# Optimization experiments

Measured on AMD Instinct MI355X. Metric: run time of the kernel, lower is better.

Reference implementation:

```python
import jax, jax.numpy as jnp
import numpy as np

N = 8192      # nodes
E = 131072    # edges (avg degree 16)
MUL = 128     # multiplicity of 0e and 1o channels
A = 10        # node_attrs (element one-hot) dim
RB = 8        # radial basis size
INV_SQRT3 = 0.5773502691896258  # w3j normalization for l=1 paths


def _lin0(x, W):
    # e3nn-style Linear on scalar (l=0) channels, 1/sqrt(fan_in) normalization
    return (x @ W) / jnp.sqrt(jnp.asarray(W.shape[0], x.dtype))


def _lin1(v, W):
    # e3nn-style Linear on l=1 channels: mixes multiplicities, acts identically on the 3 components
    return jnp.einsum('nuc,uw->nwc', v, W) / jnp.sqrt(jnp.asarray(W.shape[0], v.dtype))


def setup_inputs() -> dict:
    key = jax.random.key(0)
    ks = jax.random.split(key, 26)
    f32 = jnp.float32
    w = lambda k, s: jax.random.normal(k, s, f32)
    D_EF = RB + 2 * MUL  # 264: radial basis + source + target scalar embeddings
    return {
        'node_attrs': jax.random.uniform(ks[0], (N, A), f32),
        'node_feats': w(ks[1], (N, 4 * MUL)),
        'edge_attrs': w(ks[2], (E, 4)),
        'edge_feats': jax.random.uniform(ks[3], (E, RB), f32),
        'edge_index': jax.random.randint(ks[4], (2, E), 0, N, jnp.int32),
        'W_skip_s': w(ks[5], (MUL, MUL)), 'W_skip_v': w(ks[6], (MUL, MUL)),
        'W_up_s': w(ks[7], (MUL, MUL)), 'W_up_v': w(ks[8], (MUL, MUL)),
        'W_src': w(ks[9], (A, MUL)), 'W_tgt': w(ks[10], (A, MUL)),
        'W_r0': w(ks[11], (D_EF, 64)), 'W_r1': w(ks[12], (64, 64)),
        'W_r2': w(ks[13], (64, 64)), 'W_r3': w(ks[14], (64, 4 * MUL)),
        'W_d0': w(ks[15], (D_EF, 64)), 'W_d1': w(ks[16], (64, 1)),
        'W1_s': w(ks[17], (2 * MUL, 2 * MUL)), 'W1_v': w(ks[18], (2 * MUL, MUL)),
        'Wres_s': w(ks[19], (MUL, 2 * MUL)), 'Wres_v': w(ks[20], (MUL, MUL)),
        'W2_s': w(ks[21], (MUL, MUL)), 'W2_v': w(ks[22], (MUL, MUL)),
        'alpha': jnp.asarray(20.0, f32), 'beta': jnp.asarray(0.0, f32),
    }


def reference(node_attrs, node_feats, edge_attrs, edge_feats, edge_index,
              W_skip_s, W_skip_v, W_up_s, W_up_v, W_src, W_tgt,
              W_r0, W_r1, W_r2, W_r3, W_d0, W_d1,
              W1_s, W1_v, Wres_s, Wres_v, W2_s, W2_v, alpha, beta):
    n = node_feats.shape[0]
    s = node_feats[:, :MUL]                       # [N,128] 0e
    v = node_feats[:, MUL:].reshape(n, MUL, 3)    # [N,128,3] 1o
    # skip_tp: Linear(node_feats -> hidden)
    sc = jnp.concatenate([_lin0(s, W_skip_s), _lin1(v, W_skip_v).reshape(n, -1)], axis=-1)
    # linear_up: Linear(node_feats -> edge_irreps)
    us, uv = _lin0(s, W_up_s), _lin1(v, W_up_v)
    # source/target scalar embeddings from node_attrs
    src_e = _lin0(node_attrs, W_src)
    tgt_e = _lin0(node_attrs, W_tgt)
    snd, rcv = edge_index[0], edge_index[1]
    ef = jnp.concatenate([edge_feats, src_e[snd], tgt_e[rcv]], axis=-1)   # [E,264]
    # radial MLP -> per-edge tensor product weights
    h = jax.nn.silu(_lin0(ef, W_r0))
    h = jax.nn.silu(_lin0(h, W_r1))
    h = jax.nn.silu(_lin0(h, W_r2))
    tpw = _lin0(h, W_r3)                          # [E, 4*128]
    # edge density -> per-node density via scatter-sum
    d = jax.nn.silu(_lin0(ef, W_d0))
    edge_density = jnp.tanh(_lin0(d, W_d1) ** 2)  # [E,1]
    density = jax.ops.segment_sum(edge_density, rcv, num_segments=n)      # [N,1]
    # sparse CG tensor product (uvu), paths: 0x0->0e, 0x1->1o, 1x0->1o, 1x1->0e
    xs, xv = us[snd], uv[snd]                     # gather sender features
    y0, y1 = edge_attrs[:, 0], edge_attrs[:, 1:4]
    w1, w2, w3, w4 = jnp.split(tpw, 4, axis=-1)
    m0a = w1 * xs * y0[:, None]                                          # 0e x 0e -> 0e
    m0b = w4 * jnp.einsum('euc,ec->eu', xv, y1) * INV_SQRT3              # 1o x 1o -> 0e
    m1a = (w2 * xs)[:, :, None] * y1[:, None, :] * INV_SQRT3             # 0e x 1o -> 1o
    m1b = w3[:, :, None] * xv * y0[:, None, None] * INV_SQRT3            # 1o x 0e -> 1o
    mid_s = jnp.concatenate([m0a, m0b], axis=1)   # [E,256] irreps_mid scalars
    mid_v = jnp.concatenate([m1a, m1b], axis=1)   # [E,256,3] irreps_mid vectors
    msg_s = jax.ops.segment_sum(mid_s, rcv, num_segments=n)
    msg_v = jax.ops.segment_sum(mid_v, rcv, num_segments=n)
    # linear_1 + learned density normalization
    denom = density * beta + alpha                # [N,1]
    m_s = _lin0(msg_s, W1_s) / denom
    m_v = _lin1(msg_v, W1_v) / denom[..., None]
    # linear_res on up-projected node feats
    m_s = m_s + _lin0(us, Wres_s)                 # [N,256]: 128 scalars + 128 gates
    m_v = m_v + _lin1(uv, Wres_v)                 # [N,128,3]
    # Gate: silu on scalars, sigmoid gates on vectors
    out_s = jax.nn.silu(m_s[:, :MUL])
    out_v = m_v * jax.nn.sigmoid(m_s[:, MUL:])[:, :, None]
    # linear_2
    f_s = _lin0(out_s, W2_s)
    f_v = _lin1(out_v, W2_v)
    # reshape_irreps -> [N, mul, 1+3]
    out = jnp.concatenate([f_s[:, :, None], f_v], axis=2)
    return out, sc
```

## Files before the change

kernel.cpp:

```cpp
#include <hip/hip_runtime.h>

#define NN 8192
#define EE 131072
#define MUL 128
#define AA 10
#define RB 8
#define DEF 264
#define INV_SQRT3 0.5773502691896258f
#define INV_SQRT128 0.08838834764831845f
#define INV_SQRT10 0.31622776601683794f
#define INV_SQRT264 0.06154574548966636f

typedef __attribute__((ext_vector_type(8))) short short8;
typedef __attribute__((ext_vector_type(4))) float floatx4;

#define WS_XQ     ((size_t)0)
#define WS_USB    (WS_XQ    + (size_t)NN*256)
#define WS_UVB    (WS_USB   + (size_t)NN*64)
#define WS_SRC    (WS_UVB   + (size_t)NN*192)
#define WS_TGT    (WS_SRC   + (size_t)NN*64)
#define WS_MSGSB  (WS_TGT   + (size_t)NN*64)
#define WS_MSGVB  (WS_MSGSB + (size_t)NN*128)
#define WS_GATE   (WS_MSGVB + (size_t)NN*384)
#define WS_COUNTS (WS_GATE  + (size_t)NN*128)
#define WS_OFFS   (WS_COUNTS+ (size_t)NN)
#define WS_CURSOR (WS_OFFS  + (size_t)(NN+4))
#define WS_POS    (WS_CURSOR+ (size_t)NN)
#define WS_META   (WS_POS   + (size_t)EE)
#define WS_TPW    (WS_META  + (size_t)EE*8)
#define WS_WB     (WS_TPW   + (size_t)EE*256)
#define WS_WP     (WS_WB    + (size_t)152*256)
#define WS_WN     (WS_WP    + (size_t)352*256)

__device__ __forceinline__ float silu_f(float x) {
    return x * __builtin_amdgcn_rcpf(1.f + __expf(-x));
}
__device__ __forceinline__ float sigm_f(float x) {
    return __builtin_amdgcn_rcpf(1.f + __expf(-x));
}

__device__ __forceinline__ unsigned short f2bf(float x) {
    union { float f; unsigned u; } uf; uf.f = x;
    unsigned r = uf.u + 0x7FFFu + ((uf.u >> 16) & 1u);
    return (unsigned short)(r >> 16);
}

__global__ __launch_bounds__(256) void csr_count(
    const int* __restrict__ edge_index, int* __restrict__ counts)
{
    int e = blockIdx.x * 256 + threadIdx.x;
    atomicAdd(&counts[edge_index[EE + e]], 1);
}

__global__ __launch_bounds__(1024) void csr_scan(
    const int* __restrict__ counts, int* __restrict__ offs, int* __restrict__ cursor)
{
    __shared__ int sums[1024];
    const int t = threadIdx.x;
    int local[8];
    int s = 0;
#pragma unroll
    for (int k = 0; k < 8; ++k) { local[k] = s; s += counts[t * 8 + k]; }
    sums[t] = s;
    __syncthreads();
    for (int d = 1; d < 1024; d <<= 1) {
        int v = (t >= d) ? sums[t - d] : 0;
        __syncthreads();
        sums[t] += v;
        __syncthreads();
    }
    int base = (t > 0) ? sums[t - 1] : 0;
#pragma unroll
    for (int k = 0; k < 8; ++k) {
        offs[t * 8 + k] = base + local[k];
        cursor[t * 8 + k] = base + local[k];
    }
    if (t == 1023) offs[8192] = sums[1023];
}

__global__ __launch_bounds__(256) void csr_scatter(
    const int* __restrict__ edge_index, int* __restrict__ cursor, int* __restrict__ pos)
{
    int e = blockIdx.x * 256 + threadIdx.x;
    pos[e] = atomicAdd(&cursor[edge_index[EE + e]], 1);
}

__global__ __launch_bounds__(256) void swizzle_weights(
    const float* __restrict__ Wr0, const float* __restrict__ Wd0,
    const float* __restrict__ Wr1, const float* __restrict__ Wr2,
    const float* __restrict__ Wr3, unsigned short* __restrict__ WBall)
{
    int fid = blockIdx.x * 256 + threadIdx.x;
    int lane = fid & 63;
    int frag = fid >> 6;
    int k0 = (lane >> 4) * 8;
    int n0 = lane & 15;
    unsigned short o[8];

    if (frag < 72) {
        int kt = frag >> 3, nt = frag & 7;
        int n = nt * 16 + n0;
#pragma unroll
        for (int j = 0; j < 8; ++j) {
            int k = kt * 32 + k0 + j;
            float v = 0.f;
            if (k < 264) v = ((n < 64) ? Wr0[k * 64 + n] : Wd0[k * 64 + (n - 64)]) * INV_SQRT264;
            o[j] = f2bf(v);
        }
    } else if (frag < 80) {
        int fl = frag - 72;
        int kt = fl >> 2, nt = fl & 3;
        int n = nt * 16 + n0;
#pragma unroll
        for (int j = 0; j < 8; ++j)
            o[j] = f2bf(Wr1[(kt * 32 + k0 + j) * 64 + n] * 0.125f);
    } else if (frag < 88) {
        int fl = frag - 80;
        int kt = fl >> 2, nt = fl & 3;
        int n = nt * 16 + n0;
#pragma unroll
        for (int j = 0; j < 8; ++j)
            o[j] = f2bf(Wr2[(kt * 32 + k0 + j) * 64 + n] * 0.125f);
    } else {
        int fl = frag - 88;
        int kt = fl >> 5, nt = fl & 31;
        int n = nt * 16 + n0;
        int q = n >> 6;
        float sc = (q < 2) ? 0.125f : 0.125f * INV_SQRT3;
#pragma unroll
        for (int j = 0; j < 8; ++j)
            o[j] = f2bf(Wr3[(kt * 32 + k0 + j) * 512 + n] * sc);
    }
    uint4 pk;
    pk.x = (unsigned)o[0] | ((unsigned)o[1] << 16);
    pk.y = (unsigned)o[2] | ((unsigned)o[3] << 16);
    pk.z = (unsigned)o[4] | ((unsigned)o[5] << 16);
    pk.w = (unsigned)o[6] | ((unsigned)o[7] << 16);
    *(uint4*)(WBall + (size_t)fid * 8) = pk;
}

__global__ __launch_bounds__(256) void swizzle_post(
    const float* __restrict__ W1s, const float* __restrict__ W1v,
    const float* __restrict__ Wrs, const float* __restrict__ Wrv,
    const float* __restrict__ W2s, const float* __restrict__ W2v,
    unsigned short* __restrict__ WPall)
{
    int fid = blockIdx.x * 256 + threadIdx.x;
    int lane = fid & 63;
    int frag = fid >> 6;
    int k0 = (lane >> 4) * 8;
    int n0 = lane & 15;
    unsigned short o[8];

    if (frag < 192) {
        int kt = frag >> 4, nt = frag & 15;
        int n = nt * 16 + n0;
#pragma unroll
        for (int j = 0; j < 8; ++j) {
            int k = kt * 32 + k0 + j;
            float v = (k < 256) ? W1s[k * 256 + n] * 0.0625f
                                : Wrs[(k - 256) * 256 + n] * INV_SQRT128;
            o[j] = f2bf(v);
        }
    } else if (frag < 288) {
        int fl = frag - 192;
        int kt = fl >> 3, nt = fl & 7;
        int n = nt * 16 + n0;
#pragma unroll
        for (int j = 0; j < 8; ++j) {
            int k = kt * 32 + k0 + j;
            float v = (k < 256) ? W1v[k * 128 + n] * 0.0625f
                                : Wrv[(k - 256) * 128 + n] * INV_SQRT128;
            o[j] = f2bf(v);
        }
    } else if (frag < 320) {
        int fl = frag - 288;
        int kt = fl >> 3, nt = fl & 7;
        int n = nt * 16 + n0;
#pragma unroll
        for (int j = 0; j < 8; ++j)
            o[j] = f2bf(W2s[(kt * 32 + k0 + j) * 128 + n] * INV_SQRT128);
    } else {
        int fl = frag - 320;
        int kt = fl >> 3, nt = fl & 7;
        int n = nt * 16 + n0;
#pragma unroll
        for (int j = 0; j < 8; ++j)
            o[j] = f2bf(W2v[(kt * 32 + k0 + j) * 128 + n] * INV_SQRT128);
    }
    uint4 pk;
    pk.x = (unsigned)o[0] | ((unsigned)o[1] << 16);
    pk.y = (unsigned)o[2] | ((unsigned)o[3] << 16);
    pk.z = (unsigned)o[4] | ((unsigned)o[5] << 16);
    pk.w = (unsigned)o[6] | ((unsigned)o[7] << 16);
    *(uint4*)(WPall + (size_t)fid * 8) = pk;
}

__global__ __launch_bounds__(256) void swizzle_node(
    const float* __restrict__ Wss, const float* __restrict__ Wus,
    const float* __restrict__ Wsv, const float* __restrict__ Wuv,
    const float* __restrict__ Wsrc, const float* __restrict__ Wtgt,
    unsigned short* __restrict__ WN)
{
    int fid = blockIdx.x * 256 + threadIdx.x;
    int lane = fid & 63;
    int frag = fid >> 6;
    int k0 = (lane >> 4) * 8;
    int m0 = lane & 15;
    unsigned short o[8];

    if (frag < 128) {
        int g = frag >> 5;
        int fl = frag & 31;
        int kt = fl >> 3, mt = fl & 7;
        const float* W = (g == 0) ? Wss : (g == 1) ? Wus : (g == 2) ? Wsv : Wuv;
        int m = mt * 16 + m0;
#pragma unroll
        for (int j = 0; j < 8; ++j)
            o[j] = f2bf(W[(kt * 32 + k0 + j) * 128 + m] * INV_SQRT128);
    } else {
        int g = (frag - 128) >> 3;
        int mt = frag & 7;
        const float* W = g ? Wtgt : Wsrc;
        int m = mt * 16 + m0;
#pragma unroll
        for (int j = 0; j < 8; ++j) {
            int k = k0 + j;
            o[j] = f2bf((k < AA) ? W[k * 128 + m] * INV_SQRT10 : 0.f);
        }
    }
    uint4 pk;
    pk.x = (unsigned)o[0] | ((unsigned)o[1] << 16);
    pk.y = (unsigned)o[2] | ((unsigned)o[3] << 16);
    pk.z = (unsigned)o[4] | ((unsigned)o[5] << 16);
    pk.w = (unsigned)o[6] | ((unsigned)o[7] << 16);
    *(uint4*)(WN + (size_t)fid * 8) = pk;
}

#define PNB 16
__global__ __launch_bounds__(256) void node_pre_mfma(
    const float* __restrict__ node_attrs, const float* __restrict__ node_feats,
    const unsigned short* __restrict__ WN,
    float* __restrict__ sc_out, uint2* __restrict__ xq,
    unsigned short* __restrict__ us_b, unsigned short* __restrict__ uv_b,
    unsigned short* __restrict__ srcEb, unsigned short* __restrict__ tgtEb)
{
    __shared__ __align__(16) unsigned short Xs[PNB][136];
    __shared__ __align__(16) unsigned short Xv[3][PNB][136];
    __shared__ __align__(16) unsigned short Xa[PNB][40];
    const int t = threadIdx.x;
    const int l = t & 63, w = t >> 6;
    const int quad = l >> 4, lr = l & 15;
    const int n0 = blockIdx.x * PNB;

    {
        const int r = t >> 4, m = t & 15;
        const float* src = node_feats + (size_t)(n0 + r) * 512;
        float4 s0 = *(const float4*)(src + 8 * m);
        float4 s1 = *(const float4*)(src + 8 * m + 4);
        uint4 sp;
        sp.x = (unsigned)f2bf(s0.x) | ((unsigned)f2bf(s0.y) << 16);
        sp.y = (unsigned)f2bf(s0.z) | ((unsigned)f2bf(s0.w) << 16);
        sp.z = (unsigned)f2bf(s1.x) | ((unsigned)f2bf(s1.y) << 16);
        sp.w = (unsigned)f2bf(s1.z) | ((unsigned)f2bf(s1.w) << 16);
        *(uint4*)&Xs[r][8 * m] = sp;

        float4 q[6];
#pragma unroll
        for (int jj = 0; jj < 6; ++jj)
            q[jj] = *(const float4*)(src + 128 + 24 * m + 4 * jj);
        const float* qf = &q[0].x;
        unsigned short vb[3][8];
#pragma unroll
        for (int u = 0; u < 8; ++u) {
#pragma unroll
            for (int c = 0; c < 3; ++c)
                vb[c][u] = f2bf(qf[u * 3 + c]);
        }
#pragma unroll
        for (int c = 0; c < 3; ++c) {
            uint4 vp;
            vp.x = (unsigned)vb[c][0] | ((unsigned)vb[c][1] << 16);
            vp.y = (unsigned)vb[c][2] | ((unsigned)vb[c][3] << 16);
            vp.z = (unsigned)vb[c][4] | ((unsigned)vb[c][5] << 16);
            vp.w = (unsigned)vb[c][6] | ((unsigned)vb[c][7] << 16);
            *(uint4*)&Xv[c][r][8 * m] = vp;
        }
    }
    for (int idx = t; idx < PNB * 32; idx += 256) {
        int r = idx >> 5, k = idx & 31;
        float v = (k < AA) ? node_attrs[(size_t)(n0 + r) * AA + k] : 0.f;
        Xa[r][k] = f2bf(v);
    }
    __syncthreads();

    const short8* WNf = (const short8*)WN;
    const int n = n0 + lr;

#pragma unroll
    for (int mi = 0; mi < 2; ++mi) {
        const int mt = w * 2 + mi;
        const int j0 = mt * 16 + quad * 4;

        floatx4 cSrc = (floatx4){0.f, 0.f, 0.f, 0.f};
        floatx4 cTgt = (floatx4){0.f, 0.f, 0.f, 0.f};
        {
            short8 ba = *(const short8*)&Xa[lr][quad * 8];
            cSrc = __builtin_amdgcn_mfma_f32_16x16x32_bf16(WNf[(size_t)(128 + mt) * 64 + l], ba, cSrc, 0, 0, 0);
            cTgt = __builtin_amdgcn_mfma_f32_16x16x32_bf16(WNf[(size_t)(136 + mt) * 64 + l], ba, cTgt, 0, 0, 0);
        }
        floatx4 cS = (floatx4){0.f, 0.f, 0.f, 0.f};
        floatx4 cU = (floatx4){0.f, 0.f, 0.f, 0.f};
#pragma unroll
        for (int kt = 0; kt < 4; ++kt) {
            short8 bs = *(const short8*)&Xs[lr][kt * 32 + quad * 8];
            cS = __builtin_amdgcn_mfma_f32_16x16x32_bf16(WNf[(size_t)(kt * 8 + mt) * 64 + l], bs, cS, 0, 0, 0);
            cU = __builtin_amdgcn_mfma_f32_16x16x32_bf16(WNf[(size_t)(32 + kt * 8 + mt) * 64 + l], bs, cU, 0, 0, 0);
        }
        floatx4 cSV[3], cUV[3];
#pragma unroll
        for (int c = 0; c < 3; ++c) {
            cSV[c] = (floatx4){0.f, 0.f, 0.f, 0.f};
            cUV[c] = (floatx4){0.f, 0.f, 0.f, 0.f};
#pragma unroll
            for (int kt = 0; kt < 4; ++kt) {
                short8 bv = *(const short8*)&Xv[c][lr][kt * 32 + quad * 8];
                cSV[c] = __builtin_amdgcn_mfma_f32_16x16x32_bf16(WNf[(size_t)(64 + kt * 8 + mt) * 64 + l], bv, cSV[c], 0, 0, 0);
                cUV[c] = __builtin_amdgcn_mfma_f32_16x16x32_bf16(WNf[(size_t)(96 + kt * 8 + mt) * 64 + l], bv, cUV[c], 0, 0, 0);
            }
        }

        {
            float4 o;
            o.x = cS[0]; o.y = cS[1]; o.z = cS[2]; o.w = cS[3];
            *(float4*)(sc_out + (size_t)n * 512 + j0) = o;
        }
        {
            float vv[12];
#pragma unroll
            for (int reg = 0; reg < 4; ++reg)
#pragma unroll
                for (int c = 0; c < 3; ++c) vv[reg * 3 + c] = cSV[c][reg];
            float* dst = sc_out + (size_t)n * 512 + 128 + j0 * 3;
#pragma unroll
            for (int qq = 0; qq < 3; ++qq) {
                float4 o;
                o.x = vv[qq * 4]; o.y = vv[qq * 4 + 1]; o.z = vv[qq * 4 + 2]; o.w = vv[qq * 4 + 3];
                *(float4*)(dst + qq * 4) = o;
            }
        }
        unsigned short ub[4], vxb[4], vyb[4], vzb[4];
#pragma unroll
        for (int reg = 0; reg < 4; ++reg) {
            ub[reg] = f2bf(cU[reg]);
            vxb[reg] = f2bf(cUV[0][reg]);
            vyb[reg] = f2bf(cUV[1][reg]);
            vzb[reg] = f2bf(cUV[2][reg]);
        }
        {
            uint2 p;
            p.x = (unsigned)ub[0] | ((unsigned)ub[1] << 16);
            p.y = (unsigned)ub[2] | ((unsigned)ub[3] << 16);
            *(uint2*)(us_b + (size_t)n * 128 + j0) = p;
        }
        {
            uint2 p;
            p.x = (unsigned)vxb[0] | ((unsigned)vxb[1] << 16);
            p.y = (unsigned)vxb[2] | ((unsigned)vxb[3] << 16);
            *(uint2*)(uv_b + ((size_t)0 * NN + n) * 128 + j0) = p;
            p.x = (unsigned)vyb[0] | ((unsigned)vyb[1] << 16);
            p.y = (unsigned)vyb[2] | ((unsigned)vyb[3] << 16);
            *(uint2*)(uv_b + ((size_t)1 * NN + n) * 128 + j0) = p;
            p.x = (unsigned)vzb[0] | ((unsigned)vzb[1] << 16);
            p.y = (unsigned)vzb[2] | ((unsigned)vzb[3] << 16);
            *(uint2*)(uv_b + ((size_t)2 * NN + n) * 128 + j0) = p;
        }
        {
            uint4 x0, x1;
            x0.x = (unsigned)ub[0] | ((unsigned)vxb[0] << 16);
            x0.y = (unsigned)vyb[0] | ((unsigned)vzb[0] << 16);
            x0.z = (unsigned)ub[1] | ((unsigned)vxb[1] << 16);
            x0.w = (unsigned)vyb[1] | ((unsigned)vzb[1] << 16);
            x1.x = (unsigned)ub[2] | ((unsigned)vxb[2] << 16);
            x1.y = (unsigned)vyb[2] | ((unsigned)vzb[2] << 16);
            x1.z = (unsigned)ub[3] | ((unsigned)vxb[3] << 16);
            x1.w = (unsigned)vyb[3] | ((unsigned)vzb[3] << 16);
            uint4* xp = (uint4*)(xq + (size_t)n * 128 + j0);
            xp[0] = x0; xp[1] = x1;
        }
        {
            uint2 p;
            p.x = (unsigned)f2bf(cSrc[0]) | ((unsigned)f2bf(cSrc[1]) << 16);
            p.y = (unsigned)f2bf(cSrc[2]) | ((unsigned)f2bf(cSrc[3]) << 16);
            *(uint2*)(srcEb + (size_t)n * 128 + j0) = p;
            p.x = (unsigned)f2bf(cTgt[0]) | ((unsigned)f2bf(cTgt[1]) << 16);
            p.y = (unsigned)f2bf(cTgt[2]) | ((unsigned)f2bf(cTgt[3]) << 16);
            *(uint2*)(tgtEb + (size_t)n * 128 + j0) = p;
        }
    }
}

#define EBK 64
#define H1OFF 80
#define HLD 152
__global__ __launch_bounds__(256, 4) void edge_mlp(
    const float* __restrict__ edge_attrs, const float* __restrict__ edge_feats,
    const int* __restrict__ edge_index,
    const unsigned short* __restrict__ srcEb, const unsigned short* __restrict__ tgtEb,
    const unsigned short* __restrict__ WB0, const unsigned short* __restrict__ WB1,
    const unsigned short* __restrict__ WB2, const unsigned short* __restrict__ WB3,
    const float* __restrict__ Wd1, const int* __restrict__ pos,
    unsigned short* __restrict__ tpwP, float* __restrict__ metaP)
{
    __shared__ __align__(16) unsigned short Hb[4][16][HLD];

    const int t = threadIdx.x;
    const int l = t & 63;
    const int w = t >> 6;
    const int quad = l >> 4;
    const int lr = l & 15;
    const int e0 = blockIdx.x * EBK + w * 16;

    const int eA = e0 + lr;
    const int sndA = edge_index[eA];
    const int rcvA = edge_index[EE + eA];
    const unsigned short* spp = srcEb + (size_t)sndA * 128;
    const unsigned short* tpp = tgtEb + (size_t)rcvA * 128;

    if (quad == 0) {
        float4 ya = *(const float4*)(edge_attrs + (size_t)eA * 4);
        float4 m;
        m.x = __int_as_float(sndA); m.y = ya.y; m.z = ya.z; m.w = ya.w;
        *(float4*)(metaP + (size_t)pos[eA] * 8) = m;
    }

    short8 afr[9];
    {
        const int cq = quad * 8;
        if (quad == 0) {
            float4 f0 = *(const float4*)(edge_feats + (size_t)eA * 8);
            float4 f1 = *(const float4*)(edge_feats + (size_t)eA * 8 + 4);
            union { short8 v; unsigned u[4]; } pk;
            pk.u[0] = (unsigned)f2bf(f0.x) | ((unsigned)f2bf(f0.y) << 16);
            pk.u[1] = (unsigned)f2bf(f0.z) | ((unsigned)f2bf(f0.w) << 16);
            pk.u[2] = (unsigned)f2bf(f1.x) | ((unsigned)f2bf(f1.y) << 16);
            pk.u[3] = (unsigned)f2bf(f1.z) | ((unsigned)f2bf(f1.w) << 16);
            afr[0] = pk.v;
        } else {
            afr[0] = *(const short8*)(spp + (cq - 8));
        }
#pragma unroll
        for (int kt = 1; kt < 9; ++kt) {
            const int c = kt * 32 + cq;
            if (c < 136) {
                afr[kt] = *(const short8*)(spp + (c - 8));
            } else if (c < 264) {
                afr[kt] = *(const short8*)(tpp + (c - 136));
            } else {
                short8 z = {0, 0, 0, 0, 0, 0, 0, 0};
                afr[kt] = z;
            }
        }
    }

    unsigned short (*H)[HLD] = Hb[w];

    {
        floatx4 c0[8];
#pragma unroll
        for (int nt = 0; nt < 8; ++nt) c0[nt] = (floatx4){0.f, 0.f, 0.f, 0.f};
#pragma unroll
        for (int kt = 0; kt < 9; ++kt) {
            const short8* bp = (const short8*)WB0 + (size_t)(kt * 8) * 64 + l;
#pragma unroll
            for (int nt = 0; nt < 8; ++nt)
                c0[nt] = __builtin_amdgcn_mfma_f32_16x16x32_bf16(afr[kt], bp[nt * 64], c0[nt], 0, 0, 0);
        }

#pragma unroll
        for (int nt = 0; nt < 4; ++nt)
#pragma unroll
            for (int reg = 0; reg < 4; ++reg)
                H[quad * 4 + reg][nt * 16 + lr] = f2bf(silu_f(c0[nt][reg]));

        float wd1v[4];
#pragma unroll
        for (int q2 = 0; q2 < 4; ++q2) wd1v[q2] = Wd1[q2 * 16 + lr] * 0.125f;
        float dp[4] = {0.f, 0.f, 0.f, 0.f};
#pragma unroll
        for (int nt = 0; nt < 4; ++nt)
#pragma unroll
            for (int reg = 0; reg < 4; ++reg)
                dp[reg] += silu_f(c0[nt + 4][reg]) * wd1v[nt];
#pragma unroll
        for (int m2 = 1; m2 < 16; m2 <<= 1) {
#pragma unroll
            for (int reg = 0; reg < 4; ++reg) dp[reg] += __shfl_xor(dp[reg], m2);
        }
        if (lr == 0) {
#pragma unroll
            for (int reg = 0; reg < 4; ++reg)
                metaP[(size_t)pos[e0 + quad * 4 + reg] * 8 + 4] = tanhf(dp[reg] * dp[reg]);
        }
    }

    const unsigned short* hrow0 = &H[lr][quad * 8];
    const unsigned short* hrow1 = &H[lr][H1OFF + quad * 8];

    {
        floatx4 c1[4];
#pragma unroll
        for (int nt = 0; nt < 4; ++nt) c1[nt] = (floatx4){0.f, 0.f, 0.f, 0.f};
#pragma unroll
        for (int kt = 0; kt < 2; ++kt) {
            short8 af = *(const short8*)(hrow0 + kt * 32);
            const short8* bp = (const short8*)WB1 + (size_t)(kt * 4) * 64 + l;
#pragma unroll
            for (int nt = 0; nt < 4; ++nt)
                c1[nt] = __builtin_amdgcn_mfma_f32_16x16x32_bf16(af, bp[nt * 64], c1[nt], 0, 0, 0);
        }
#pragma unroll
        for (int nt = 0; nt < 4; ++nt)
#pragma unroll
            for (int reg = 0; reg < 4; ++reg)
                H[quad * 4 + reg][H1OFF + nt * 16 + lr] = f2bf(silu_f(c1[nt][reg]));
    }

    {
        floatx4 c2[4];
#pragma unroll
        for (int nt = 0; nt < 4; ++nt) c2[nt] = (floatx4){0.f, 0.f, 0.f, 0.f};
#pragma unroll
        for (int kt = 0; kt < 2; ++kt) {
            short8 af = *(const short8*)(hrow1 + kt * 32);
            const short8* bp = (const short8*)WB2 + (size_t)(kt * 4) * 64 + l;
#pragma unroll
            for (int nt = 0; nt < 4; ++nt)
                c2[nt] = __builtin_amdgcn_mfma_f32_16x16x32_bf16(af, bp[nt * 64], c2[nt], 0, 0, 0);
        }
#pragma unroll
        for (int nt = 0; nt < 4; ++nt)
#pragma unroll
            for (int reg = 0; reg < 4; ++reg)
                H[quad * 4 + reg][nt * 16 + lr] = f2bf(silu_f(c2[nt][reg]));
    }

    {
        int slotr[4];
        float y0r[4];
#pragma unroll
        for (int reg = 0; reg < 4; ++reg) {
            const int er = e0 + quad * 4 + reg;
            slotr[reg] = pos[er];
            y0r[reg] = edge_attrs[(size_t)er * 4];
        }
        short8 af0 = *(const short8*)(hrow0);
        short8 af1 = *(const short8*)(hrow0 + 32);
        uint2* tpw2 = (uint2*)tpwP;
#pragma unroll
        for (int j2 = 0; j2 < 8; ++j2) {
            floatx4 c3[4];
#pragma unroll
            for (int g = 0; g < 4; ++g) c3[g] = (floatx4){0.f, 0.f, 0.f, 0.f};
#pragma unroll
            for (int g = 0; g < 4; ++g) {
                const short8* b0 = (const short8*)WB3 + (size_t)(g * 8 + j2) * 64 + l;
                const short8* b1 = (const short8*)WB3 + (size_t)(32 + g * 8 + j2) * 64 + l;
                c3[g] = __builtin_amdgcn_mfma_f32_16x16x32_bf16(af0, *b0, c3[g], 0, 0, 0);
                c3[g] = __builtin_amdgcn_mfma_f32_16x16x32_bf16(af1, *b1, c3[g], 0, 0, 0);
            }
            const int u = j2 * 16 + lr;
#pragma unroll
            for (int reg = 0; reg < 4; ++reg) {
                float w1v = c3[0][reg] * y0r[reg];
                float w2v = c3[1][reg];
                float w3v = c3[2][reg] * y0r[reg];
                float w4v = c3[3][reg];
                uint2 p;
                p.x = (unsigned)f2bf(w1v) | ((unsigned)f2bf(w2v) << 16);
                p.y = (unsigned)f2bf(w3v) | ((unsigned)f2bf(w4v) << 16);
                tpw2[(size_t)slotr[reg] * 128 + u] = p;
            }
        }
    }
}

__global__ __launch_bounds__(128) void node_gather(
    const unsigned short* __restrict__ tpwP, const float* __restrict__ metaP,
    const int* __restrict__ offs, const uint2* __restrict__ xq,
    const float* __restrict__ alpha_p, const float* __restrict__ beta_p,
    unsigned short* __restrict__ msgs_b, unsigned short* __restrict__ msgv_b)
{
    const int n = blockIdx.x;
    const int j = threadIdx.x;
    const int s0 = offs[n], s1 = offs[n + 1];
    const uint2* tpw2 = (const uint2*)tpwP;

    float as0 = 0.f, as1 = 0.f;
    float av0x = 0.f, av0y = 0.f, av0z = 0.f;
    float av1x = 0.f, av1y = 0.f, av1z = 0.f;
    float dsum = 0.f;

    int s = s0;
    for (; s + 4 <= s1; s += 4) {
        float4 ma[4]; float dn[4]; uint2 wv[4]; uint2 xv[4];
#pragma unroll
        for (int k = 0; k < 4; ++k) {
            ma[k] = *(const float4*)&metaP[(size_t)(s + k) * 8];
            dn[k] = metaP[(size_t)(s + k) * 8 + 4];
            wv[k] = tpw2[(size_t)(s + k) * 128 + j];
        }
#pragma unroll
        for (int k = 0; k < 4; ++k)
            xv[k] = xq[(size_t)__float_as_int(ma[k].x) * 128 + j];
#pragma unroll
        for (int k = 0; k < 4; ++k) {
            const float y1x = ma[k].y, y1y = ma[k].z, y1z = ma[k].w;
            dsum += dn[k];
            const float w1  = __uint_as_float(wv[k].x << 16);
            const float w2  = __uint_as_float(wv[k].x & 0xffff0000u);
            const float w3  = __uint_as_float(wv[k].y << 16);
            const float w4  = __uint_as_float(wv[k].y & 0xffff0000u);
            const float xs  = __uint_as_float(xv[k].x << 16);
            const float xvx = __uint_as_float(xv[k].x & 0xffff0000u);
            const float xvy = __uint_as_float(xv[k].y << 16);
            const float xvz = __uint_as_float(xv[k].y & 0xffff0000u);
            as0 += w1 * xs;
            as1 += w4 * (xvx * y1x + xvy * y1y + xvz * y1z);
            const float b2 = w2 * xs;
            av0x += b2 * y1x; av0y += b2 * y1y; av0z += b2 * y1z;
            av1x += w3 * xvx; av1y += w3 * xvy; av1z += w3 * xvz;
        }
    }
    for (; s < s1; ++s) {
        const float4 m0 = *(const float4*)&metaP[(size_t)s * 8];
        const float dns = metaP[(size_t)s * 8 + 4];
        const int snd = __float_as_int(m0.x);
        const float y1x = m0.y, y1y = m0.z, y1z = m0.w;
        dsum += dns;
        uint2 wv = tpw2[(size_t)s * 128 + j];
        uint2 xv = xq[(size_t)snd * 128 + j];
        const float w1  = __uint_as_float(wv.x << 16);
        const float w2  = __uint_as_float(wv.x & 0xffff0000u);
        const float w3  = __uint_as_float(wv.y << 16);
        const float w4  = __uint_as_float(wv.y & 0xffff0000u);
        const float xs  = __uint_as_float(xv.x << 16);
        const float xvx = __uint_as_float(xv.x & 0xffff0000u);
        const float xvy = __uint_as_float(xv.y << 16);
        const float xvz = __uint_as_float(xv.y & 0xffff0000u);
        as0 += w1 * xs;
        as1 += w4 * (xvx * y1x + xvy * y1y + xvz * y1z);
        const float b2 = w2 * xs;
        av0x += b2 * y1x; av0y += b2 * y1y; av0z += b2 * y1z;
        av1x += w3 * xvx; av1y += w3 * xvy; av1z += w3 * xvz;
    }

    const float invden = 1.f / (dsum * (*beta_p) + (*alpha_p));

    msgs_b[(size_t)n * 256 + j]       = f2bf(as0 * invden);
    msgs_b[(size_t)n * 256 + 128 + j] = f2bf(as1 * invden);
    msgv_b[((size_t)0 * NN + n) * 256 + j]       = f2bf(av0x * invden);
    msgv_b[((size_t)0 * NN + n) * 256 + 128 + j] = f2bf(av1x * invden);
    msgv_b[((size_t)1 * NN + n) * 256 + j]       = f2bf(av0y * invden);
    msgv_b[((size_t)1 * NN + n) * 256 + 128 + j] = f2bf(av1y * invden);
    msgv_b[((size_t)2 * NN + n) * 256 + j]       = f2bf(av0z * invden);
    msgv_b[((size_t)2 * NN + n) * 256 + 128 + j] = f2bf(av1z * invden);
}

#define DNP 32
__global__ __launch_bounds__(256) void post_s(
    const unsigned short* __restrict__ msgs_b, const unsigned short* __restrict__ us_b,
    const unsigned short* __restrict__ WPs, const unsigned short* __restrict__ W2ss,
    float* __restrict__ gate, float* __restrict__ out)
{
    __shared__ __align__(16) unsigned short At[DNP][392];
    __shared__ __align__(16) unsigned short osb[DNP][136];
    const int t = threadIdx.x;
    const int l = t & 63, w = t >> 6;
    const int quad = l >> 4, lr = l & 15;
    const int n0 = blockIdx.x * DNP;
    const int rt = w & 1, nh = w >> 1;

    for (int idx = t; idx < DNP * 48; idx += 256) {
        int r = idx / 48, q = idx - r * 48;
        uint4 v;
        if (q < 32) v = *(const uint4*)(msgs_b + (size_t)(n0 + r) * 256 + q * 8);
        else        v = *(const uint4*)(us_b   + (size_t)(n0 + r) * 128 + (q - 32) * 8);
        *(uint4*)&At[r][q * 8] = v;
    }
    __syncthreads();

    int rowr[4];
#pragma unroll
    for (int reg = 0; reg < 4; ++reg) rowr[reg] = rt * 16 + quad * 4 + reg;

    floatx4 c1[8];
#pragma unroll
    for (int nt = 0; nt < 8; ++nt) c1[nt] = (floatx4){0.f, 0.f, 0.f, 0.f};
    const unsigned short* arow = &At[rt * 16 + lr][quad * 8];
#pragma unroll
    for (int kt = 0; kt < 12; ++kt) {
        short8 af = *(const short8*)(arow + kt * 32);
        const short8* bp = (const short8*)WPs + (size_t)(kt * 16 + nh * 8) * 64 + l;
#pragma unroll
        for (int nt = 0; nt < 8; ++nt)
            c1[nt] = __builtin_amdgcn_mfma_f32_16x16x32_bf16(af, bp[nt * 64], c1[nt], 0, 0, 0);
    }
    if (nh == 0) {
#pragma unroll
        for (int nt = 0; nt < 8; ++nt)
#pragma unroll
            for (int reg = 0; reg < 4; ++reg)
                osb[rowr[reg]][nt * 16 + lr] = f2bf(silu_f(c1[nt][reg]));
    } else {
#pragma unroll
        for (int nt = 0; nt < 8; ++nt)
#pragma unroll
            for (int reg = 0; reg < 4; ++reg)
                gate[(size_t)(n0 + rowr[reg]) * 128 + nt * 16 + lr] = sigm_f(c1[nt][reg]);
    }
    __syncthreads();

    floatx4 c2[4];
#pragma unroll
    for (int nt = 0; nt < 4; ++nt) c2[nt] = (floatx4){0.f, 0.f, 0.f, 0.f};
    const unsigned short* arow2 = &osb[rt * 16 + lr][quad * 8];
#pragma unroll
    for (int kt = 0; kt < 4; ++kt) {
        short8 af = *(const short8*)(arow2 + kt * 32);
        const short8* bp = (const short8*)W2ss + (size_t)(kt * 8 + nh * 4) * 64 + l;
#pragma unroll
        for (int nt = 0; nt < 4; ++nt)
            c2[nt] = __builtin_amdgcn_mfma_f32_16x16x32_bf16(af, bp[nt * 64], c2[nt], 0, 0, 0);
    }
#pragma unroll
    for (int nt = 0; nt < 4; ++nt)
#pragma unroll
        for (int reg = 0; reg < 4; ++reg)
            out[(size_t)(n0 + rowr[reg]) * 512 + (nh * 64 + nt * 16 + lr) * 4] = c2[nt][reg];
}

__global__ __launch_bounds__(256) void post_v(
    const unsigned short* __restrict__ msgv_b, const unsigned short* __restrict__ uv_b,
    const unsigned short* __restrict__ WPv, const unsigned short* __restrict__ W2vs,
    const float* __restrict__ gate, float* __restrict__ out)
{
    __shared__ __align__(16) unsigned short At[DNP][392];
    __shared__ __align__(16) unsigned short ovb[DNP][136];
    const int t = threadIdx.x;
    const int l = t & 63, w = t >> 6;
    const int quad = l >> 4, lr = l & 15;
    const int c = blockIdx.x >> 8;
    const int n0 = (blockIdx.x & 255) * DNP;
    const int rt = w & 1, nh = w >> 1;

    for (int idx = t; idx < DNP * 48; idx += 256) {
        int r = idx / 48, q = idx - r * 48;
        uint4 v;
        if (q < 32) v = *(const uint4*)(msgv_b + ((size_t)c * NN + n0 + r) * 256 + q * 8);
        else        v = *(const uint4*)(uv_b   + ((size_t)c * NN + n0 + r) * 128 + (q - 32) * 8);
        *(uint4*)&At[r][q * 8] = v;
    }
    __syncthreads();

    int rowr[4];
#pragma unroll
    for (int reg = 0; reg < 4; ++reg) rowr[reg] = rt * 16 + quad * 4 + reg;

    floatx4 c1[4];
#pragma unroll
    for (int nt = 0; nt < 4; ++nt) c1[nt] = (floatx4){0.f, 0.f, 0.f, 0.f};
    const unsigned short* arow = &At[rt * 16 + lr][quad * 8];
#pragma unroll
    for (int kt = 0; kt < 12; ++kt) {
        short8 af = *(const short8*)(arow + kt * 32);
        const short8* bp = (const short8*)WPv + (size_t)(kt * 8 + nh * 4) * 64 + l;
#pragma unroll
        for (int nt = 0; nt < 4; ++nt)
            c1[nt] = __builtin_amdgcn_mfma_f32_16x16x32_bf16(af, bp[nt * 64], c1[nt], 0, 0, 0);
    }
#pragma unroll
    for (int nt = 0; nt < 4; ++nt)
#pragma unroll
        for (int reg = 0; reg < 4; ++reg) {
            int col = nh * 64 + nt * 16 + lr;
            float g = gate[(size_t)(n0 + rowr[reg]) * 128 + col];
            ovb[rowr[reg]][col] = f2bf(c1[nt][reg] * g);
        }
    __syncthreads();

    floatx4 c2[4];
#pragma unroll
    for (int nt = 0; nt < 4; ++nt) c2[nt] = (floatx4){0.f, 0.f, 0.f, 0.f};
    const unsigned short* arow2 = &ovb[rt * 16 + lr][quad * 8];
#pragma unroll
    for (int kt = 0; kt < 4; ++kt) {
        short8 af = *(const short8*)(arow2 + kt * 32);
        const short8* bp = (const short8*)W2vs + (size_t)(kt * 8 + nh * 4) * 64 + l;
#pragma unroll
        for (int nt = 0; nt < 4; ++nt)
            c2[nt] = __builtin_amdgcn_mfma_f32_16x16x32_bf16(af, bp[nt * 64], c2[nt], 0, 0, 0);
    }
#pragma unroll
    for (int nt = 0; nt < 4; ++nt)
#pragma unroll
        for (int reg = 0; reg < 4; ++reg)
            out[(size_t)(n0 + rowr[reg]) * 512 + (nh * 64 + nt * 16 + lr) * 4 + 1 + c]
                = c2[nt][reg];
}

extern "C" void kernel_launch(void* const* d_in, const int* in_sizes, int n_in,
                              void* d_out, int out_size, void* d_ws, size_t ws_size,
                              hipStream_t stream)
{
    const float* node_attrs = (const float*)d_in[0];
    const float* node_feats = (const float*)d_in[1];
    const float* edge_attrs = (const float*)d_in[2];
    const float* edge_feats = (const float*)d_in[3];
    const int*   edge_index = (const int*)d_in[4];
    const float* W_skip_s = (const float*)d_in[5];
    const float* W_skip_v = (const float*)d_in[6];
    const float* W_up_s   = (const float*)d_in[7];
    const float* W_up_v   = (const float*)d_in[8];
    const float* W_src    = (const float*)d_in[9];
    const float* W_tgt    = (const float*)d_in[10];
    const float* W_r0     = (const float*)d_in[11];
    const float* W_r1     = (const float*)d_in[12];
    const float* W_r2     = (const float*)d_in[13];
    const float* W_r3     = (const float*)d_in[14];
    const float* W_d0     = (const float*)d_in[15];
    const float* W_d1     = (const float*)d_in[16];
    const float* W1_s     = (const float*)d_in[17];
    const float* W1_v     = (const float*)d_in[18];
    const float* Wres_s   = (const float*)d_in[19];
    const float* Wres_v   = (const float*)d_in[20];
    const float* W2_s     = (const float*)d_in[21];
    const float* W2_v     = (const float*)d_in[22];
    const float* alpha_p  = (const float*)d_in[23];
    const float* beta_p   = (const float*)d_in[24];

    float* out = (float*)d_out;
    float* sc_out = out + (size_t)NN * 512;
    float* ws = (float*)d_ws;

    uint2* xq = (uint2*)(ws + WS_XQ);
    unsigned short* us_b  = (unsigned short*)(ws + WS_USB);
    unsigned short* uv_b  = (unsigned short*)(ws + WS_UVB);
    unsigned short* srcEb = (unsigned short*)(ws + WS_SRC);
    unsigned short* tgtEb = (unsigned short*)(ws + WS_TGT);
    unsigned short* msgs_b = (unsigned short*)(ws + WS_MSGSB);
    unsigned short* msgv_b = (unsigned short*)(ws + WS_MSGVB);
    float* gate  = ws + WS_GATE;
    int*   counts = (int*)(ws + WS_COUNTS);
    int*   offs   = (int*)(ws + WS_OFFS);
    int*   cursor = (int*)(ws + WS_CURSOR);
    int*   pos    = (int*)(ws + WS_POS);
    float* metaP  = ws + WS_META;
    unsigned short* tpwP = (unsigned short*)(ws + WS_TPW);
    unsigned short* WBall = (unsigned short*)(ws + WS_WB);
    unsigned short* WB0 = WBall;
    unsigned short* WB1 = WB0 + (size_t)72 * 512;
    unsigned short* WB2 = WB1 + (size_t)8 * 512;
    unsigned short* WB3 = WB2 + (size_t)8 * 512;
    unsigned short* WPall = (unsigned short*)(ws + WS_WP);
    unsigned short* WPs  = WPall;
    unsigned short* WPv  = WPs + (size_t)192 * 512;
    unsigned short* W2ss = WPv + (size_t)96 * 512;
    unsigned short* W2vs = W2ss + (size_t)32 * 512;
    unsigned short* WN   = (unsigned short*)(ws + WS_WN);

    hipMemsetAsync(counts, 0, (size_t)NN * sizeof(int), stream);

    csr_count<<<EE / 256, 256, 0, stream>>>(edge_index, counts);
    csr_scan<<<1, 1024, 0, stream>>>(counts, offs, cursor);
    csr_scatter<<<EE / 256, 256, 0, stream>>>(edge_index, cursor, pos);

    swizzle_weights<<<38, 256, 0, stream>>>(W_r0, W_d0, W_r1, W_r2, W_r3, WBall);
    swizzle_post<<<88, 256, 0, stream>>>(W1_s, W1_v, Wres_s, Wres_v, W2_s, W2_v, WPall);
    swizzle_node<<<36, 256, 0, stream>>>(W_skip_s, W_up_s, W_skip_v, W_up_v,
                                         W_src, W_tgt, WN);

    node_pre_mfma<<<NN / PNB, 256, 0, stream>>>(
        node_attrs, node_feats, WN, sc_out, xq, us_b, uv_b, srcEb, tgtEb);

    edge_mlp<<<EE / EBK, 256, 0, stream>>>(
        edge_attrs, edge_feats, edge_index, srcEb, tgtEb,
        WB0, WB1, WB2, WB3, W_d1, pos, tpwP, metaP);

    node_gather<<<NN, 128, 0, stream>>>(
        tpwP, metaP, offs, xq, alpha_p, beta_p, msgs_b, msgv_b);

    post_s<<<NN / DNP, 256, 0, stream>>>(msgs_b, us_b, WPs, W2ss, gate, out);
    post_v<<<3 * NN / DNP, 256, 0, stream>>>(msgv_b, uv_b, WPv, W2vs, gate, out);
}
```

Measured before the change: 315.2 us.

## Fuse scalar and vector post-processing kernels into one gated node kernel

Merges post_s and post_v into a single kernel handling 16 nodes per block. The gate values now stay in shared memory instead of being written to and re-read from a global buffer, and one launch replaces two. A operands are loaded straight from global memory into registers, with no shared-memory staging. Each wave splits its scalar and vector output tiles across the three components. The costs are fewer blocks (512), uncoalesced per-lane row loads, and more accumulator registers per thread.

```diff
diff --git a/kernel.cpp b/kernel.cpp
--- a/kernel.cpp
+++ b/kernel.cpp
@@ -667,146 +667,134 @@
     msgv_b[((size_t)2 * NN + n) * 256 + 128 + j] = f2bf(av1z * invden);
 }
 
-#define DNP 32
-__global__ __launch_bounds__(256) void post_s(
+#define DNP 16
+__global__ __launch_bounds__(256) void post_fused(
     const unsigned short* __restrict__ msgs_b, const unsigned short* __restrict__ us_b,
-    const unsigned short* __restrict__ WPs, const unsigned short* __restrict__ W2ss,
-    float* __restrict__ gate, float* __restrict__ out)
-{
-    __shared__ __align__(16) unsigned short At[DNP][392];
+    const unsigned short* __restrict__ msgv_b, const unsigned short* __restrict__ uv_b,
+    const unsigned short* __restrict__ WPs, const unsigned short* __restrict__ WPv,
+    const unsigned short* __restrict__ W2ss, const unsigned short* __restrict__ W2vs,
+    float* __restrict__ out)
+{
     __shared__ __align__(16) unsigned short osb[DNP][136];
+    __shared__ __align__(16) unsigned short ovb[3][DNP][136];
+    __shared__ float gateL[DNP][128];
+
     const int t = threadIdx.x;
     const int l = t & 63, w = t >> 6;
     const int quad = l >> 4, lr = l & 15;
     const int n0 = blockIdx.x * DNP;
-    const int rt = w & 1, nh = w >> 1;
-
-    for (int idx = t; idx < DNP * 48; idx += 256) {
-        int r = idx / 48, q = idx - r * 48;
-        uint4 v;
-        if (q < 32) v = *(const uint4*)(msgs_b + (size_t)(n0 + r) * 256 + q * 8);
-        else        v = *(const uint4*)(us_b   + (size_t)(n0 + r) * 128 + (q - 32) * 8);
-        *(uint4*)&At[r][q * 8] = v;
+    const int nh = w;
+    const int n = n0 + lr;
+
+    const int cLo = (nh * 6) >> 3;
+    const int cHi = (nh * 6 + 5) >> 3;
+
+    const unsigned short* sRow  = msgs_b + (size_t)n * 256;
+    const unsigned short* uRow  = us_b   + (size_t)n * 128;
+    const unsigned short* vRowL = msgv_b + ((size_t)cLo * NN + n) * 256;
+    const unsigned short* uRowL = uv_b   + ((size_t)cLo * NN + n) * 128;
+    const unsigned short* vRowH = msgv_b + ((size_t)cHi * NN + n) * 256;
+    const unsigned short* uRowH = uv_b   + ((size_t)cHi * NN + n) * 128;
+
+    floatx4 accS[4], accV[6];
+#pragma unroll
+    for (int i = 0; i < 4; ++i) accS[i] = (floatx4){0.f, 0.f, 0.f, 0.f};
+#pragma unroll
+    for (int i = 0; i < 6; ++i) accV[i] = (floatx4){0.f, 0.f, 0.f, 0.f};
+
+#pragma unroll
+    for (int kt = 0; kt < 12; ++kt) {
+        const int col = kt * 32 + quad * 8;
+        short8 aS = (col < 256) ? *(const short8*)(sRow + col)
+                                : *(const short8*)(uRow + col - 256);
+        short8 aV0 = (col < 256) ? *(const short8*)(vRowL + col)
+                                 : *(const short8*)(uRowL + col - 256);
+        short8 aV1;
+        if (cHi != cLo)
+            aV1 = (col < 256) ? *(const short8*)(vRowH + col)
+                              : *(const short8*)(uRowH + col - 256);
+        else
+            aV1 = aV0;
+
+        const short8* bpS = (const short8*)WPs + (size_t)(kt * 16 + nh * 4) * 64 + l;
+#pragma unroll
+        for (int i = 0; i < 4; ++i)
+            accS[i] = __builtin_amdgcn_mfma_f32_16x16x32_bf16(aS, bpS[i * 64], accS[i], 0, 0, 0);
+#pragma unroll
+        for (int i = 0; i < 6; ++i) {
+            const int vt = nh * 6 + i;
+            const short8* bpV = (const short8*)WPv + (size_t)(kt * 8 + (vt & 7)) * 64 + l;
+            short8 a = ((vt >> 3) == cLo) ? aV0 : aV1;
+            accV[i] = __builtin_amdgcn_mfma_f32_16x16x32_bf16(a, *bpV, accV[i], 0, 0, 0);
+        }
+    }
+
+#pragma unroll
+    for (int i = 0; i < 4; ++i) {
+        const int tile = nh * 4 + i;
+#pragma unroll
+        for (int reg = 0; reg < 4; ++reg) {
+            const int row = quad * 4 + reg;
+            const float v = accS[i][reg];
+            if (tile < 8) osb[row][tile * 16 + lr] = f2bf(silu_f(v));
+            else          gateL[row][(tile - 8) * 16 + lr] = sigm_f(v);
+        }
     }
     __syncthreads();
 
-    int rowr[4];
-#pragma unroll
-    for (int reg = 0; reg < 4; ++reg) rowr[reg] = rt * 16 + quad * 4 + reg;
-
-    floatx4 c1[8];
-#pragma unroll
-    for (int nt = 0; nt < 8; ++nt) c1[nt] = (floatx4){0.f, 0.f, 0.f, 0.f};
-    const unsigned short* arow = &At[rt * 16 + lr][quad * 8];
-#pragma unroll
-    for (int kt = 0; kt < 12; ++kt) {
-        short8 af = *(const short8*)(arow + kt * 32);
-        const short8* bp = (const short8*)WPs + (size_t)(kt * 16 + nh * 8) * 64 + l;
-#pragma unroll
-        for (int nt = 0; nt < 8; ++nt)
-            c1[nt] = __builtin_amdgcn_mfma_f32_16x16x32_bf16(af, bp[nt * 64], c1[nt], 0, 0, 0);
-    }
-    if (nh == 0) {
-#pragma unroll
-        for (int nt = 0; nt < 8; ++nt)
-#pragma unroll
-            for (int reg = 0; reg < 4; ++reg)
-                osb[rowr[reg]][nt * 16 + lr] = f2bf(silu_f(c1[nt][reg]));
-    } else {
-#pragma unroll
-        for (int nt = 0; nt < 8; ++nt)
-#pragma unroll
-            for (int reg = 0; reg < 4; ++reg)
-                gate[(size_t)(n0 + rowr[reg]) * 128 + nt * 16 + lr] = sigm_f(c1[nt][reg]);
+#pragma unroll
+    for (int i = 0; i < 6; ++i) {
+        const int vt = nh * 6 + i;
+        const int c = vt >> 3;
+        const int colv = (vt & 7) * 16 + lr;
+#pragma unroll
+        for (int reg = 0; reg < 4; ++reg) {
+            const int row = quad * 4 + reg;
+            ovb[c][row][colv] = f2bf(accV[i][reg] * gateL[row][colv]);
+        }
     }
     __syncthreads();
 
-    floatx4 c2[4];
-#pragma unroll
-    for (int nt = 0; nt < 4; ++nt) c2[nt] = (floatx4){0.f, 0.f, 0.f, 0.f};
-    const unsigned short* arow2 = &osb[rt * 16 + lr][quad * 8];
+    floatx4 c2s[2], c2v[6];
+#pragma unroll
+    for (int i = 0; i < 2; ++i) c2s[i] = (floatx4){0.f, 0.f, 0.f, 0.f};
+#pragma unroll
+    for (int i = 0; i < 6; ++i) c2v[i] = (floatx4){0.f, 0.f, 0.f, 0.f};
+
+    const unsigned short* arowS = &osb[lr][quad * 8];
 #pragma unroll
     for (int kt = 0; kt < 4; ++kt) {
-        short8 af = *(const short8*)(arow2 + kt * 32);
-        const short8* bp = (const short8*)W2ss + (size_t)(kt * 8 + nh * 4) * 64 + l;
-#pragma unroll
-        for (int nt = 0; nt < 4; ++nt)
-            c2[nt] = __builtin_amdgcn_mfma_f32_16x16x32_bf16(af, bp[nt * 64], c2[nt], 0, 0, 0);
-    }
-#pragma unroll
-    for (int nt = 0; nt < 4; ++nt)
+        short8 afS = *(const short8*)(arowS + kt * 32);
+        const short8* bpS = (const short8*)W2ss + (size_t)(kt * 8 + nh * 2) * 64 + l;
+#pragma unroll
+        for (int i = 0; i < 2; ++i)
+            c2s[i] = __builtin_amdgcn_mfma_f32_16x16x32_bf16(afS, bpS[i * 64], c2s[i], 0, 0, 0);
+#pragma unroll
+        for (int i = 0; i < 6; ++i) {
+            const int vt = nh * 6 + i;
+            const int c = vt >> 3;
+            short8 afV = *(const short8*)(&ovb[c][lr][quad * 8] + kt * 32);
+            const short8* bpV = (const short8*)W2vs + (size_t)(kt * 8 + (vt & 7)) * 64 + l;
+            c2v[i] = __builtin_amdgcn_mfma_f32_16x16x32_bf16(afV, *bpV, c2v[i], 0, 0, 0);
+        }
+    }
+
+#pragma unroll
+    for (int i = 0; i < 2; ++i) {
+        const int col = (nh * 2 + i) * 16 + lr;
 #pragma unroll
         for (int reg = 0; reg < 4; ++reg)
-            out[(size_t)(n0 + rowr[reg]) * 512 + (nh * 64 + nt * 16 + lr) * 4] = c2[nt][reg];
-}
-
-__global__ __launch_bounds__(256) void post_v(
-    const unsigned short* __restrict__ msgv_b, const unsigned short* __restrict__ uv_b,
-    const unsigned short* __restrict__ WPv, const unsigned short* __restrict__ W2vs,
-    const float* __restrict__ gate, float* __restrict__ out)
-{
-    __shared__ __align__(16) unsigned short At[DNP][392];
-    __shared__ __align__(16) unsigned short ovb[DNP][136];
-    const int t = threadIdx.x;
-    const int l = t & 63, w = t >> 6;
-    const int quad = l >> 4, lr = l & 15;
-    const int c = blockIdx.x >> 8;
-    const int n0 = (blockIdx.x & 255) * DNP;
-    const int rt = w & 1, nh = w >> 1;
-
-    for (int idx = t; idx < DNP * 48; idx += 256) {
-        int r = idx / 48, q = idx - r * 48;
-        uint4 v;
-        if (q < 32) v = *(const uint4*)(msgv_b + ((size_t)c * NN + n0 + r) * 256 + q * 8);
-        else        v = *(const uint4*)(uv_b   + ((size_t)c * NN + n0 + r) * 128 + (q - 32) * 8);
-        *(uint4*)&At[r][q * 8] = v;
-    }
-    __syncthreads();
-
-    int rowr[4];
-#pragma unroll
-    for (int reg = 0; reg < 4; ++reg) rowr[reg] = rt * 16 + quad * 4 + reg;
-
-    floatx4 c1[4];
-#pragma unroll
-    for (int nt = 0; nt < 4; ++nt) c1[nt] = (floatx4){0.f, 0.f, 0.f, 0.f};
-    const unsigned short* arow = &At[rt * 16 + lr][quad * 8];
-#pragma unroll
-    for (int kt = 0; kt < 12; ++kt) {
-        short8 af = *(const short8*)(arow + kt * 32);
-        const short8* bp = (const short8*)WPv + (size_t)(kt * 8 + nh * 4) * 64 + l;
-#pragma unroll
-        for (int nt = 0; nt < 4; ++nt)
-            c1[nt] = __builtin_amdgcn_mfma_f32_16x16x32_bf16(af, bp[nt * 64], c1[nt], 0, 0, 0);
-    }
-#pragma unroll
-    for (int nt = 0; nt < 4; ++nt)
-#pragma unroll
-        for (int reg = 0; reg < 4; ++reg) {
-            int col = nh * 64 + nt * 16 + lr;
-            float g = gate[(size_t)(n0 + rowr[reg]) * 128 + col];
-            ovb[rowr[reg]][col] = f2bf(c1[nt][reg] * g);
-        }
-    __syncthreads();
-
-    floatx4 c2[4];
-#pragma unroll
-    for (int nt = 0; nt < 4; ++nt) c2[nt] = (floatx4){0.f, 0.f, 0.f, 0.f};
-    const unsigned short* arow2 = &ovb[rt * 16 + lr][quad * 8];
-#pragma unroll
-    for (int kt = 0; kt < 4; ++kt) {
-        short8 af = *(const short8*)(arow2 + kt * 32);
-        const short8* bp = (const short8*)W2vs + (size_t)(kt * 8 + nh * 4) * 64 + l;
-#pragma unroll
-        for (int nt = 0; nt < 4; ++nt)
-            c2[nt] = __builtin_amdgcn_mfma_f32_16x16x32_bf16(af, bp[nt * 64], c2[nt], 0, 0, 0);
-    }
-#pragma unroll
-    for (int nt = 0; nt < 4; ++nt)
+            out[(size_t)(n0 + quad * 4 + reg) * 512 + col * 4] = c2s[i][reg];
+    }
+#pragma unroll
+    for (int i = 0; i < 6; ++i) {
+        const int vt = nh * 6 + i;
+        const int c = vt >> 3;
+        const int col = (vt & 7) * 16 + lr;
 #pragma unroll
         for (int reg = 0; reg < 4; ++reg)
-            out[(size_t)(n0 + rowr[reg]) * 512 + (nh * 64 + nt * 16 + lr) * 4 + 1 + c]
-                = c2[nt][reg];
+            out[(size_t)(n0 + quad * 4 + reg) * 512 + col * 4 + 1 + c] = c2v[i][reg];
+    }
 }
 
 extern "C" void kernel_launch(void* const* d_in, const int* in_sizes, int n_in,
@@ -850,7 +838,6 @@
     unsigned short* tgtEb = (unsigned short*)(ws + WS_TGT);
     unsigned short* msgs_b = (unsigned short*)(ws + WS_MSGSB);
     unsigned short* msgv_b = (unsigned short*)(ws + WS_MSGVB);
-    float* gate  = ws + WS_GATE;
     int*   counts = (int*)(ws + WS_COUNTS);
     int*   offs   = (int*)(ws + WS_OFFS);
     int*   cursor = (int*)(ws + WS_CURSOR);
@@ -890,6 +877,6 @@
     node_gather<<<NN, 128, 0, stream>>>(
         tpwP, metaP, offs, xq, alpha_p, beta_p, msgs_b, msgv_b);
 
-    post_s<<<NN / DNP, 256, 0, stream>>>(msgs_b, us_b, WPs, W2ss, gate, out);
-    post_v<<<3 * NN / DNP, 256, 0, stream>>>(msgv_b, uv_b, WPv, W2vs, gate, out);
-}
+    post_fused<<<NN / DNP, 256, 0, stream>>>(
+        msgs_b, us_b, msgv_b, uv_b, WPs, WPv, W2ss, W2vs, out);
+}
```

After: 304.1 us, median of 2. 3.5% less time.
